# Kernel optimization log

Hardware: AMD Instinct MI355X
Metric: run time of the kernel (lower is better)

Reference implementation:

```python
import jax, jax.numpy as jnp
import numpy as np

NUM_NODES = 5000
NUM_COLORS = 20
NODE_FEAT = 4
COLOR_FEAT = 3
COMBINED = NODE_FEAT + COLOR_FEAT  # 7
HIDDEN = 128
N_GRAPH = NUM_NODES * NUM_COLORS   # 100000 GCN nodes (batch=1)
N_EDGES = 1_600_000


def setup_inputs() -> dict:
    key = jax.random.key(0)
    ks = jax.random.split(key, 12)
    flat_obs = jax.random.normal(ks[0], (1, 3 + NUM_NODES * NODE_FEAT + NUM_COLORS * COLOR_FEAT), dtype=jnp.float32)
    edge_index = jax.random.randint(ks[1], (2, N_EDGES), 0, N_GRAPH, dtype=jnp.int64)
    s = lambda k, sh, fan: jax.random.normal(k, sh, dtype=jnp.float32) / np.sqrt(fan)
    return {
        "flat_obs": flat_obs,
        "edge_index": edge_index,
        "W1": s(ks[2], (COMBINED, HIDDEN), COMBINED),
        "b1": jnp.zeros((HIDDEN,), jnp.float32),
        "W2": s(ks[3], (HIDDEN, HIDDEN), HIDDEN),
        "b2": jnp.zeros((HIDDEN,), jnp.float32),
        "fc1_w": s(ks[4], (HIDDEN, HIDDEN), HIDDEN),
        "fc1_b": jnp.zeros((HIDDEN,), jnp.float32),
        "fc2_w": s(ks[5], (HIDDEN, 1), HIDDEN),
        "fc2_b": jnp.zeros((1,), jnp.float32),
    }


def _gcn_conv(x, W, b, src, dst, norm):
    # PyG GCNConv: out[dst] += norm * (x @ W)[src]; self-loops already in src/dst.
    xw = x @ W                                   # [N, H]
    msg = xw[src] * norm[:, None]                # [E+N, H]
    out = jax.ops.segment_sum(msg, dst, num_segments=N_GRAPH)
    return out + b


def reference(flat_obs, edge_index, W1, b1, W2, b2, fc1_w, fc1_b, fc2_w, fc2_b):
    B = flat_obs.shape[0]
    nf_start = 3
    nf_end = nf_start + NUM_NODES * NODE_FEAT
    cf_end = nf_end + NUM_COLORS * COLOR_FEAT
    node_features = flat_obs[:, nf_start:nf_end].reshape(B, NUM_NODES, NODE_FEAT)
    color_features = flat_obs[:, nf_end:cf_end].reshape(B, NUM_COLORS, COLOR_FEAT)

    # cross-expand: [B, nodes, colors, 4+3]
    en = jnp.broadcast_to(node_features[:, :, None, :], (B, NUM_NODES, NUM_COLORS, NODE_FEAT))
    ec = jnp.broadcast_to(color_features[:, None, :, :], (B, NUM_NODES, NUM_COLORS, COLOR_FEAT))
    combined = jnp.concatenate([en, ec], axis=3).reshape(-1, COMBINED)  # [N_GRAPH, 7]

    # add self loops + symmetric normalization (GCN)
    loops = jnp.arange(N_GRAPH, dtype=edge_index.dtype)
    src = jnp.concatenate([edge_index[0], loops])
    dst = jnp.concatenate([edge_index[1], loops])
    deg = jax.ops.segment_sum(jnp.ones_like(dst, dtype=jnp.float32), dst, num_segments=N_GRAPH)
    dinv = jnp.where(deg > 0, jax.lax.rsqrt(deg), 0.0)
    norm = dinv[src] * dinv[dst]

    x = jax.nn.relu(_gcn_conv(combined, W1, b1, src, dst, norm))
    x = jax.nn.relu(_gcn_conv(x, W2, b2, src, dst, norm))
    x = jax.nn.relu(x @ fc1_w + fc1_b)
    q = x @ fc2_w + fc2_b                         # [N_GRAPH, 1]
    return q.reshape(B, NUM_NODES * NUM_COLORS)
```

## Files before the change

### kernel.cpp

```cpp
#include <hip/hip_runtime.h>

#define NGRAPH 100000
#define NEDGE  1600000
#define HID    128
#define SCAN_B 512
#define NBLK   ((NGRAPH + SCAN_B - 1) / SCAN_B)
#define TILE   32

__device__ __forceinline__ int e_src(const int* ei, int is64, int e) {
    return is64 ? ei[2 * e] : ei[e];
}
__device__ __forceinline__ int e_dst(const int* ei, int is64, int e) {
    return is64 ? ei[2 * NEDGE + 2 * e] : ei[NEDGE + e];
}

__global__ void k_prep(const float* __restrict__ obs, const int* __restrict__ ei,
                       float* __restrict__ comb, int* __restrict__ deg,
                       int* __restrict__ fill, int* __restrict__ flag) {
    if (blockIdx.x == 0 && threadIdx.x < 64) {
        int v = ei[2 * threadIdx.x + 1];
        unsigned long long b = __ballot(v != 0);
        if (threadIdx.x == 0) flag[0] = (b == 0ull) ? 1 : 0;
    }
    int i = blockIdx.x * blockDim.x + threadIdx.x;
    if (i >= NGRAPH) return;
    int n = i / 20, c = i % 20;
    const float* nf = obs + 3 + n * 4;
    const float* cf = obs + 3 + 20000 + c * 3;
    float* o = comb + i * 7;
    o[0] = nf[0]; o[1] = nf[1]; o[2] = nf[2]; o[3] = nf[3];
    o[4] = cf[0]; o[5] = cf[1]; o[6] = cf[2];
    deg[i] = 0;
    fill[i] = 0;
}

__global__ void k_deg(const int* __restrict__ ei, const int* __restrict__ flag,
                      int* __restrict__ deg) {
    int e = blockIdx.x * blockDim.x + threadIdx.x;
    if (e >= NEDGE) return;
    atomicAdd(&deg[e_dst(ei, flag[0], e)], 1);
}

__global__ void __launch_bounds__(SCAN_B) k_scan1(const int* __restrict__ deg,
                                                  int* __restrict__ rowptr,
                                                  int* __restrict__ sums,
                                                  float* __restrict__ dinv) {
    __shared__ int sh[SCAN_B];
    int t = threadIdx.x;
    int i = blockIdx.x * SCAN_B + t;
    int val = (i < NGRAPH) ? deg[i] : 0;
    if (i < NGRAPH) dinv[i] = rsqrtf((float)(val + 1));
    sh[t] = val;
    __syncthreads();
    for (int o = 1; o < SCAN_B; o <<= 1) {
        int x = (t >= o) ? sh[t - o] : 0;
        __syncthreads();
        sh[t] += x;
        __syncthreads();
    }
    if (i < NGRAPH) rowptr[i] = sh[t] - val;
    if (t == SCAN_B - 1) sums[blockIdx.x] = sh[t];
}

__global__ void __launch_bounds__(256) k_scan2(int* __restrict__ sums) {
    __shared__ int sh[256];
    int t = threadIdx.x;
    int val = (t < NBLK) ? sums[t] : 0;
    sh[t] = val;
    __syncthreads();
    for (int o = 1; o < 256; o <<= 1) {
        int x = (t >= o) ? sh[t - o] : 0;
        __syncthreads();
        sh[t] += x;
        __syncthreads();
    }
    if (t < NBLK) sums[t] = sh[t] - val;
}

__global__ void __launch_bounds__(SCAN_B) k_scan3(int* __restrict__ rowptr,
                                                  const int* __restrict__ sums) {
    int i = blockIdx.x * SCAN_B + threadIdx.x;
    if (i < NGRAPH) rowptr[i] += sums[blockIdx.x];
}

__global__ void k_fill(const int* __restrict__ ei, const int* __restrict__ flag,
                       const float* __restrict__ dinv,
                       const int* __restrict__ rowptr, int* __restrict__ fill,
                       int* __restrict__ csr_src, float* __restrict__ csr_w) {
    int e = blockIdx.x * blockDim.x + threadIdx.x;
    if (e >= NEDGE) return;
    int is64 = flag[0];
    int s = e_src(ei, is64, e);
    int d = e_dst(ei, is64, e);
    int pos = rowptr[d] + atomicAdd(&fill[d], 1);
    csr_src[pos] = s;
    csr_w[pos] = dinv[s] * dinv[d];
}

__global__ void __launch_bounds__(256) k_gcn1(const int* __restrict__ rowptr,
                                              const int* __restrict__ deg,
                                              const int* __restrict__ csr_src,
                                              const float* __restrict__ csr_w,
                                              const float* __restrict__ dinv,
                                              const float* __restrict__ comb,
                                              const float* __restrict__ W1,
                                              const float* __restrict__ b1,
                                              float* __restrict__ x1) {
    __shared__ float agg_s[32][8];
    int g = threadIdx.x >> 3;
    int f = threadIdx.x & 7;
    int d = blockIdx.x * 32 + g;
    if (f < 7) {
        int start = rowptr[d], n = deg[d];
        float acc = 0.0f;
        for (int j = 0; j < n; ++j) {
            int s = csr_src[start + j];
            float w = csr_w[start + j];
            acc += w * comb[s * 7 + f];
        }
        float dv = dinv[d];
        acc += dv * dv * comb[d * 7 + f];
        agg_s[g][f] = acc;
    }
    __syncthreads();
    float a[7];
    #pragma unroll
    for (int q = 0; q < 7; ++q) a[q] = agg_s[g][q];
    int h0 = f * 16;
    #pragma unroll
    for (int j = 0; j < 4; ++j) {
        int h = h0 + j * 4;
        float4 acc4 = *reinterpret_cast<const float4*>(b1 + h);
        #pragma unroll
        for (int q = 0; q < 7; ++q) {
            float4 w = *reinterpret_cast<const float4*>(W1 + q * HID + h);
            acc4.x += a[q] * w.x;
            acc4.y += a[q] * w.y;
            acc4.z += a[q] * w.z;
            acc4.w += a[q] * w.w;
        }
        acc4.x = fmaxf(acc4.x, 0.0f); acc4.y = fmaxf(acc4.y, 0.0f);
        acc4.z = fmaxf(acc4.z, 0.0f); acc4.w = fmaxf(acc4.w, 0.0f);
        *reinterpret_cast<float4*>(x1 + (size_t)d * HID + h) = acc4;
    }
}

__global__ void __launch_bounds__(256) k_agg2(const int* __restrict__ rowptr,
                                              const int* __restrict__ deg,
                                              const int* __restrict__ csr_src,
                                              const float* __restrict__ csr_w,
                                              const float* __restrict__ dinv,
                                              const float* __restrict__ x1,
                                              float* __restrict__ agg2) {
    int wave = threadIdx.x >> 6;
    int lane = threadIdx.x & 63;
    int d = blockIdx.x * 4 + wave;
    int f0 = lane * 2;
    int start = rowptr[d], n = deg[d];
    float2 acc = {0.0f, 0.0f};
    int j = 0;
    for (; j + 2 <= n; j += 2) {
        int s0 = csr_src[start + j];
        int s1 = csr_src[start + j + 1];
        float w0 = csr_w[start + j];
        float w1 = csr_w[start + j + 1];
        float2 v0 = *reinterpret_cast<const float2*>(x1 + (size_t)s0 * HID + f0);
        float2 v1 = *reinterpret_cast<const float2*>(x1 + (size_t)s1 * HID + f0);
        acc.x += w0 * v0.x + w1 * v1.x;
        acc.y += w0 * v0.y + w1 * v1.y;
    }
    if (j < n) {
        int s0 = csr_src[start + j];
        float w0 = csr_w[start + j];
        float2 v0 = *reinterpret_cast<const float2*>(x1 + (size_t)s0 * HID + f0);
        acc.x += w0 * v0.x;
        acc.y += w0 * v0.y;
    }
    float dv = dinv[d];
    float ws = dv * dv;
    float2 v = *reinterpret_cast<const float2*>(x1 + (size_t)d * HID + f0);
    acc.x += ws * v.x;
    acc.y += ws * v.y;
    *reinterpret_cast<float2*>(agg2 + (size_t)d * HID + f0) = acc;
}

__device__ __forceinline__ void fma4(float4& acc, const float4 a,
                                     const float4 w0, const float4 w1,
                                     const float4 w2, const float4 w3) {
    acc.x += a.x * w0.x + a.y * w1.x + a.z * w2.x + a.w * w3.x;
    acc.y += a.x * w0.y + a.y * w1.y + a.z * w2.y + a.w * w3.y;
    acc.z += a.x * w0.z + a.y * w1.z + a.z * w2.z + a.w * w3.z;
    acc.w += a.x * w0.w + a.y * w1.w + a.z * w2.w + a.w * w3.w;
}
__device__ __forceinline__ float4 relu4(float4 v) {
    float4 r;
    r.x = fmaxf(v.x, 0.0f); r.y = fmaxf(v.y, 0.0f);
    r.z = fmaxf(v.z, 0.0f); r.w = fmaxf(v.w, 0.0f);
    return r;
}

__global__ void __launch_bounds__(256) k_mlp(const float* __restrict__ agg2,
                                             const float* __restrict__ W2,
                                             const float* __restrict__ b2,
                                             const float* __restrict__ fc1w,
                                             const float* __restrict__ fc1b,
                                             const float* __restrict__ fc2w,
                                             const float* __restrict__ fc2b,
                                             float* __restrict__ out) {
    __shared__ float as_[TILE][HID + 4];
    __shared__ float ws[32][HID + 4];
    const int tid = threadIdx.x;
    const int tx = tid & 31;
    const int ty = tid >> 5;
    const int n0 = blockIdx.x * TILE;
    const int h0 = tx * 4;

    {
        const float* src = agg2 + (size_t)n0 * HID;
        #pragma unroll
        for (int q = 0; q < 4; ++q) {
            int idx = (q * 256 + tid) * 4;
            int row = idx >> 7, col = idx & 127;
            *reinterpret_cast<float4*>(&as_[row][col]) =
                *reinterpret_cast<const float4*>(src + idx);
        }
    }

    float4 bias = *reinterpret_cast<const float4*>(b2 + h0);
    float4 c0 = bias, c1 = bias, c2 = bias, c3 = bias;
    for (int ks = 0; ks < HID; ks += 32) {
        const float* wsrc = W2 + (size_t)ks * HID;
        #pragma unroll
        for (int q = 0; q < 4; ++q) {
            int idx = (q * 256 + tid) * 4;
            int row = idx >> 7, col = idx & 127;
            *reinterpret_cast<float4*>(&ws[row][col]) =
                *reinterpret_cast<const float4*>(wsrc + idx);
        }
        __syncthreads();
        #pragma unroll 4
        for (int k = 0; k < 32; k += 4) {
            float4 w0 = *reinterpret_cast<const float4*>(&ws[k + 0][h0]);
            float4 w1 = *reinterpret_cast<const float4*>(&ws[k + 1][h0]);
            float4 w2 = *reinterpret_cast<const float4*>(&ws[k + 2][h0]);
            float4 w3 = *reinterpret_cast<const float4*>(&ws[k + 3][h0]);
            float4 a0 = *reinterpret_cast<const float4*>(&as_[ty * 4 + 0][ks + k]);
            float4 a1 = *reinterpret_cast<const float4*>(&as_[ty * 4 + 1][ks + k]);
            float4 a2 = *reinterpret_cast<const float4*>(&as_[ty * 4 + 2][ks + k]);
            float4 a3 = *reinterpret_cast<const float4*>(&as_[ty * 4 + 3][ks + k]);
            fma4(c0, a0, w0, w1, w2, w3);
            fma4(c1, a1, w0, w1, w2, w3);
            fma4(c2, a2, w0, w1, w2, w3);
            fma4(c3, a3, w0, w1, w2, w3);
        }
        __syncthreads();
    }
    *reinterpret_cast<float4*>(&as_[ty * 4 + 0][h0]) = relu4(c0);
    *reinterpret_cast<float4*>(&as_[ty * 4 + 1][h0]) = relu4(c1);
    *reinterpret_cast<float4*>(&as_[ty * 4 + 2][h0]) = relu4(c2);
    *reinterpret_cast<float4*>(&as_[ty * 4 + 3][h0]) = relu4(c3);

    float4 bias1 = *reinterpret_cast<const float4*>(fc1b + h0);
    float4 d0 = bias1, d1 = bias1, d2 = bias1, d3 = bias1;
    for (int ks = 0; ks < HID; ks += 32) {
        const float* wsrc = fc1w + (size_t)ks * HID;
        #pragma unroll
        for (int q = 0; q < 4; ++q) {
            int idx = (q * 256 + tid) * 4;
            int row = idx >> 7, col = idx & 127;
            *reinterpret_cast<float4*>(&ws[row][col]) =
                *reinterpret_cast<const float4*>(wsrc + idx);
        }
        __syncthreads();
        #pragma unroll 4
        for (int k = 0; k < 32; k += 4) {
            float4 w0 = *reinterpret_cast<const float4*>(&ws[k + 0][h0]);
            float4 w1 = *reinterpret_cast<const float4*>(&ws[k + 1][h0]);
            float4 w2 = *reinterpret_cast<const float4*>(&ws[k + 2][h0]);
            float4 w3 = *reinterpret_cast<const float4*>(&ws[k + 3][h0]);
            float4 a0 = *reinterpret_cast<const float4*>(&as_[ty * 4 + 0][ks + k]);
            float4 a1 = *reinterpret_cast<const float4*>(&as_[ty * 4 + 1][ks + k]);
            float4 a2 = *reinterpret_cast<const float4*>(&as_[ty * 4 + 2][ks + k]);
            float4 a3 = *reinterpret_cast<const float4*>(&as_[ty * 4 + 3][ks + k]);
            fma4(d0, a0, w0, w1, w2, w3);
            fma4(d1, a1, w0, w1, w2, w3);
            fma4(d2, a2, w0, w1, w2, w3);
            fma4(d3, a3, w0, w1, w2, w3);
        }
        __syncthreads();
    }

    float4 wq = *reinterpret_cast<const float4*>(fc2w + h0);
    float4 r0 = relu4(d0), r1 = relu4(d1), r2 = relu4(d2), r3 = relu4(d3);
    float p0 = r0.x * wq.x + r0.y * wq.y + r0.z * wq.z + r0.w * wq.w;
    float p1 = r1.x * wq.x + r1.y * wq.y + r1.z * wq.z + r1.w * wq.w;
    float p2 = r2.x * wq.x + r2.y * wq.y + r2.z * wq.z + r2.w * wq.w;
    float p3 = r3.x * wq.x + r3.y * wq.y + r3.z * wq.z + r3.w * wq.w;
    #pragma unroll
    for (int m = 1; m < 32; m <<= 1) {
        p0 += __shfl_xor(p0, m);
        p1 += __shfl_xor(p1, m);
        p2 += __shfl_xor(p2, m);
        p3 += __shfl_xor(p3, m);
    }
    if (tx == 0) {
        float bq = fc2b[0];
        int nb = n0 + ty * 4;
        out[nb + 0] = p0 + bq;
        out[nb + 1] = p1 + bq;
        out[nb + 2] = p2 + bq;
        out[nb + 3] = p3 + bq;
    }
}

extern "C" void kernel_launch(void* const* d_in, const int* in_sizes, int n_in,
                              void* d_out, int out_size, void* d_ws, size_t ws_size,
                              hipStream_t stream) {
    const float* obs  = (const float*)d_in[0];
    const int*   ei   = (const int*)d_in[1];
    const float* W1   = (const float*)d_in[2];
    const float* b1   = (const float*)d_in[3];
    const float* W2   = (const float*)d_in[4];
    const float* b2   = (const float*)d_in[5];
    const float* fc1w = (const float*)d_in[6];
    const float* fc1b = (const float*)d_in[7];
    const float* fc2w = (const float*)d_in[8];
    const float* fc2b = (const float*)d_in[9];
    float* out = (float*)d_out;

    char* base = (char*)d_ws;
    size_t off = 0;
    auto take = [&](size_t bytes) {
        char* p = base + off;
        off += (bytes + 255) & ~(size_t)255;
        return p;
    };
    int*   deg     = (int*)take((size_t)NGRAPH * 4);
    int*   rowptr  = (int*)take((size_t)NGRAPH * 4);
    int*   fill    = (int*)take((size_t)NGRAPH * 4);
    int*   sums    = (int*)take((size_t)NBLK * 4);
    float* dinv    = (float*)take((size_t)NGRAPH * 4);
    int*   csr_src = (int*)take((size_t)NEDGE * 4);
    float* csr_w   = (float*)take((size_t)NEDGE * 4);
    float* comb    = (float*)take((size_t)NGRAPH * 7 * 4);
    float* x1      = (float*)take((size_t)NGRAPH * HID * 4);
    float* agg2    = (float*)take((size_t)NGRAPH * HID * 4);
    int*   flag    = (int*)take(256);

    k_prep<<<(NGRAPH + 255) / 256, 256, 0, stream>>>(obs, ei, comb, deg, fill, flag);
    k_deg<<<(NEDGE + 255) / 256, 256, 0, stream>>>(ei, flag, deg);
    k_scan1<<<NBLK, SCAN_B, 0, stream>>>(deg, rowptr, sums, dinv);
    k_scan2<<<1, 256, 0, stream>>>(sums);
    k_scan3<<<NBLK, SCAN_B, 0, stream>>>(rowptr, sums);
    k_fill<<<(NEDGE + 255) / 256, 256, 0, stream>>>(ei, flag, dinv, rowptr, fill,
                                                    csr_src, csr_w);
    k_gcn1<<<NGRAPH / 32, 256, 0, stream>>>(rowptr, deg, csr_src, csr_w, dinv,
                                            comb, W1, b1, x1);
    k_agg2<<<NGRAPH / 4, 256, 0, stream>>>(rowptr, deg, csr_src, csr_w, dinv,
                                           x1, agg2);
    k_mlp<<<NGRAPH / TILE, 256, 0, stream>>>(agg2, W2, b2, fc1w, fc1b,
                                             fc2w, fc2b, out);
}
```

Measured before the change: 546.2 us.

## Interleave CSR src/weight into int2 and retile MLP kernel to 64 rows

Packs each edge's source index and normalization weight into a single int2, so the gather loops in both aggregation kernels issue one 8-byte load per edge instead of two scattered 4-byte loads. The MLP kernel now processes 64 rows per block, with each thread computing 8 output columns for 4 rows, to raise register-level reuse of the shared-memory weight tiles. It also sets a launch-bounds occupancy hint and adds tail guards. The cost is more registers and shared memory per block, which could lower occupancy.

```diff
diff --git a/kernel.cpp b/kernel.cpp
--- a/kernel.cpp
+++ b/kernel.cpp
@@ -5,7 +5,7 @@
 #define HID    128
 #define SCAN_B 512
 #define NBLK   ((NGRAPH + SCAN_B - 1) / SCAN_B)
-#define TILE   32
+#define TILE   64
 
 __device__ __forceinline__ int e_src(const int* ei, int is64, int e) {
     return is64 ? ei[2 * e] : ei[e];
@@ -86,21 +86,19 @@
 __global__ void k_fill(const int* __restrict__ ei, const int* __restrict__ flag,
                        const float* __restrict__ dinv,
                        const int* __restrict__ rowptr, int* __restrict__ fill,
-                       int* __restrict__ csr_src, float* __restrict__ csr_w) {
+                       int2* __restrict__ csr) {
     int e = blockIdx.x * blockDim.x + threadIdx.x;
     if (e >= NEDGE) return;
     int is64 = flag[0];
     int s = e_src(ei, is64, e);
     int d = e_dst(ei, is64, e);
     int pos = rowptr[d] + atomicAdd(&fill[d], 1);
-    csr_src[pos] = s;
-    csr_w[pos] = dinv[s] * dinv[d];
+    csr[pos] = make_int2(s, __float_as_int(dinv[s] * dinv[d]));
 }
 
 __global__ void __launch_bounds__(256) k_gcn1(const int* __restrict__ rowptr,
                                               const int* __restrict__ deg,
-                                              const int* __restrict__ csr_src,
-                                              const float* __restrict__ csr_w,
+                                              const int2* __restrict__ csr,
                                               const float* __restrict__ dinv,
                                               const float* __restrict__ comb,
                                               const float* __restrict__ W1,
@@ -114,9 +112,8 @@
         int start = rowptr[d], n = deg[d];
         float acc = 0.0f;
         for (int j = 0; j < n; ++j) {
-            int s = csr_src[start + j];
-            float w = csr_w[start + j];
-            acc += w * comb[s * 7 + f];
+            int2 ed = csr[start + j];
+            acc += __int_as_float(ed.y) * comb[ed.x * 7 + f];
         }
         float dv = dinv[d];
         acc += dv * dv * comb[d * 7 + f];
@@ -134,10 +131,10 @@
         #pragma unroll
         for (int q = 0; q < 7; ++q) {
             float4 w = *reinterpret_cast<const float4*>(W1 + q * HID + h);
-            acc4.x += a[q] * w.x;
-            acc4.y += a[q] * w.y;
-            acc4.z += a[q] * w.z;
-            acc4.w += a[q] * w.w;
+            acc4.x = fmaf(a[q], w.x, acc4.x);
+            acc4.y = fmaf(a[q], w.y, acc4.y);
+            acc4.z = fmaf(a[q], w.z, acc4.z);
+            acc4.w = fmaf(a[q], w.w, acc4.w);
         }
         acc4.x = fmaxf(acc4.x, 0.0f); acc4.y = fmaxf(acc4.y, 0.0f);
         acc4.z = fmaxf(acc4.z, 0.0f); acc4.w = fmaxf(acc4.w, 0.0f);
@@ -147,8 +144,7 @@
 
 __global__ void __launch_bounds__(256) k_agg2(const int* __restrict__ rowptr,
                                               const int* __restrict__ deg,
-                                              const int* __restrict__ csr_src,
-                                              const float* __restrict__ csr_w,
+                                              const int2* __restrict__ csr,
                                               const float* __restrict__ dinv,
                                               const float* __restrict__ x1,
                                               float* __restrict__ agg2) {
@@ -160,19 +156,19 @@
     float2 acc = {0.0f, 0.0f};
     int j = 0;
     for (; j + 2 <= n; j += 2) {
-        int s0 = csr_src[start + j];
-        int s1 = csr_src[start + j + 1];
-        float w0 = csr_w[start + j];
-        float w1 = csr_w[start + j + 1];
-        float2 v0 = *reinterpret_cast<const float2*>(x1 + (size_t)s0 * HID + f0);
-        float2 v1 = *reinterpret_cast<const float2*>(x1 + (size_t)s1 * HID + f0);
+        int2 e0 = csr[start + j];
+        int2 e1 = csr[start + j + 1];
+        float w0 = __int_as_float(e0.y);
+        float w1 = __int_as_float(e1.y);
+        float2 v0 = *reinterpret_cast<const float2*>(x1 + (size_t)e0.x * HID + f0);
+        float2 v1 = *reinterpret_cast<const float2*>(x1 + (size_t)e1.x * HID + f0);
         acc.x += w0 * v0.x + w1 * v1.x;
         acc.y += w0 * v0.y + w1 * v1.y;
     }
     if (j < n) {
-        int s0 = csr_src[start + j];
-        float w0 = csr_w[start + j];
-        float2 v0 = *reinterpret_cast<const float2*>(x1 + (size_t)s0 * HID + f0);
+        int2 e0 = csr[start + j];
+        float w0 = __int_as_float(e0.y);
+        float2 v0 = *reinterpret_cast<const float2*>(x1 + (size_t)e0.x * HID + f0);
         acc.x += w0 * v0.x;
         acc.y += w0 * v0.y;
     }
@@ -184,13 +180,11 @@
     *reinterpret_cast<float2*>(agg2 + (size_t)d * HID + f0) = acc;
 }
 
-__device__ __forceinline__ void fma4(float4& acc, const float4 a,
-                                     const float4 w0, const float4 w1,
-                                     const float4 w2, const float4 w3) {
-    acc.x += a.x * w0.x + a.y * w1.x + a.z * w2.x + a.w * w3.x;
-    acc.y += a.x * w0.y + a.y * w1.y + a.z * w2.y + a.w * w3.y;
-    acc.z += a.x * w0.z + a.y * w1.z + a.z * w2.z + a.w * w3.z;
-    acc.w += a.x * w0.w + a.y * w1.w + a.z * w2.w + a.w * w3.w;
+__device__ __forceinline__ void fmad(float4& acc, float s, const float4 w) {
+    acc.x = fmaf(s, w.x, acc.x);
+    acc.y = fmaf(s, w.y, acc.y);
+    acc.z = fmaf(s, w.z, acc.z);
+    acc.w = fmaf(s, w.w, acc.w);
 }
 __device__ __forceinline__ float4 relu4(float4 v) {
     float4 r;
@@ -199,117 +193,133 @@
     return r;
 }
 
-__global__ void __launch_bounds__(256) k_mlp(const float* __restrict__ agg2,
-                                             const float* __restrict__ W2,
-                                             const float* __restrict__ b2,
-                                             const float* __restrict__ fc1w,
-                                             const float* __restrict__ fc1b,
-                                             const float* __restrict__ fc2w,
-                                             const float* __restrict__ fc2b,
-                                             float* __restrict__ out) {
+__global__ void __launch_bounds__(256, 3) k_mlp(const float* __restrict__ agg2,
+                                                const float* __restrict__ W2,
+                                                const float* __restrict__ b2,
+                                                const float* __restrict__ fc1w,
+                                                const float* __restrict__ fc1b,
+                                                const float* __restrict__ fc2w,
+                                                const float* __restrict__ fc2b,
+                                                float* __restrict__ out) {
     __shared__ float as_[TILE][HID + 4];
     __shared__ float ws[32][HID + 4];
     const int tid = threadIdx.x;
-    const int tx = tid & 31;
-    const int ty = tid >> 5;
+    const int tx = tid & 15;
+    const int ty = tid >> 4;
     const int n0 = blockIdx.x * TILE;
-    const int h0 = tx * 4;
-
+    const int h0 = tx * 8;
+
+    #pragma unroll
+    for (int q = 0; q < 8; ++q) {
+        int idx = (q * 256 + tid) * 4;
+        int row = idx >> 7, col = idx & 127;
+        int nr = n0 + row; if (nr >= NGRAPH) nr = NGRAPH - 1;
+        *reinterpret_cast<float4*>(&as_[row][col]) =
+            *reinterpret_cast<const float4*>(agg2 + (size_t)nr * HID + col);
+    }
+
+    float4 cA[4], cB[4];
     {
-        const float* src = agg2 + (size_t)n0 * HID;
-        #pragma unroll
-        for (int q = 0; q < 4; ++q) {
-            int idx = (q * 256 + tid) * 4;
-            int row = idx >> 7, col = idx & 127;
-            *reinterpret_cast<float4*>(&as_[row][col]) =
-                *reinterpret_cast<const float4*>(src + idx);
-        }
-    }
-
-    float4 bias = *reinterpret_cast<const float4*>(b2 + h0);
-    float4 c0 = bias, c1 = bias, c2 = bias, c3 = bias;
+        float4 bA = *reinterpret_cast<const float4*>(b2 + h0);
+        float4 bB = *reinterpret_cast<const float4*>(b2 + h0 + 4);
+        #pragma unroll
+        for (int r = 0; r < 4; ++r) { cA[r] = bA; cB[r] = bB; }
+    }
     for (int ks = 0; ks < HID; ks += 32) {
-        const float* wsrc = W2 + (size_t)ks * HID;
         #pragma unroll
         for (int q = 0; q < 4; ++q) {
             int idx = (q * 256 + tid) * 4;
             int row = idx >> 7, col = idx & 127;
             *reinterpret_cast<float4*>(&ws[row][col]) =
-                *reinterpret_cast<const float4*>(wsrc + idx);
-        }
-        __syncthreads();
-        #pragma unroll 4
+                *reinterpret_cast<const float4*>(W2 + (size_t)(ks + row) * HID + col);
+        }
+        __syncthreads();
+        #pragma unroll
         for (int k = 0; k < 32; k += 4) {
-            float4 w0 = *reinterpret_cast<const float4*>(&ws[k + 0][h0]);
-            float4 w1 = *reinterpret_cast<const float4*>(&ws[k + 1][h0]);
-            float4 w2 = *reinterpret_cast<const float4*>(&ws[k + 2][h0]);
-            float4 w3 = *reinterpret_cast<const float4*>(&ws[k + 3][h0]);
-            float4 a0 = *reinterpret_cast<const float4*>(&as_[ty * 4 + 0][ks + k]);
-            float4 a1 = *reinterpret_cast<const float4*>(&as_[ty * 4 + 1][ks + k]);
-            float4 a2 = *reinterpret_cast<const float4*>(&as_[ty * 4 + 2][ks + k]);
-            float4 a3 = *reinterpret_cast<const float4*>(&as_[ty * 4 + 3][ks + k]);
-            fma4(c0, a0, w0, w1, w2, w3);
-            fma4(c1, a1, w0, w1, w2, w3);
-            fma4(c2, a2, w0, w1, w2, w3);
-            fma4(c3, a3, w0, w1, w2, w3);
-        }
-        __syncthreads();
-    }
-    *reinterpret_cast<float4*>(&as_[ty * 4 + 0][h0]) = relu4(c0);
-    *reinterpret_cast<float4*>(&as_[ty * 4 + 1][h0]) = relu4(c1);
-    *reinterpret_cast<float4*>(&as_[ty * 4 + 2][h0]) = relu4(c2);
-    *reinterpret_cast<float4*>(&as_[ty * 4 + 3][h0]) = relu4(c3);
-
-    float4 bias1 = *reinterpret_cast<const float4*>(fc1b + h0);
-    float4 d0 = bias1, d1 = bias1, d2 = bias1, d3 = bias1;
+            float4 wA0 = *reinterpret_cast<const float4*>(&ws[k + 0][h0]);
+            float4 wB0 = *reinterpret_cast<const float4*>(&ws[k + 0][h0 + 4]);
+            float4 wA1 = *reinterpret_cast<const float4*>(&ws[k + 1][h0]);
+            float4 wB1 = *reinterpret_cast<const float4*>(&ws[k + 1][h0 + 4]);
+            float4 wA2 = *reinterpret_cast<const float4*>(&ws[k + 2][h0]);
+            float4 wB2 = *reinterpret_cast<const float4*>(&ws[k + 2][h0 + 4]);
+            float4 wA3 = *reinterpret_cast<const float4*>(&ws[k + 3][h0]);
+            float4 wB3 = *reinterpret_cast<const float4*>(&ws[k + 3][h0 + 4]);
+            #pragma unroll
+            for (int r = 0; r < 4; ++r) {
+                float4 a = *reinterpret_cast<const float4*>(&as_[ty * 4 + r][ks + k]);
+                fmad(cA[r], a.x, wA0); fmad(cB[r], a.x, wB0);
+                fmad(cA[r], a.y, wA1); fmad(cB[r], a.y, wB1);
+                fmad(cA[r], a.z, wA2); fmad(cB[r], a.z, wB2);
+                fmad(cA[r], a.w, wA3); fmad(cB[r], a.w, wB3);
+            }
+        }
+        __syncthreads();
+    }
+    #pragma unroll
+    for (int r = 0; r < 4; ++r) {
+        *reinterpret_cast<float4*>(&as_[ty * 4 + r][h0])     = relu4(cA[r]);
+        *reinterpret_cast<float4*>(&as_[ty * 4 + r][h0 + 4]) = relu4(cB[r]);
+    }
+
+    float4 dA[4], dB[4];
+    {
+        float4 bA = *reinterpret_cast<const float4*>(fc1b + h0);
+        float4 bB = *reinterpret_cast<const float4*>(fc1b + h0 + 4);
+        #pragma unroll
+        for (int r = 0; r < 4; ++r) { dA[r] = bA; dB[r] = bB; }
+    }
     for (int ks = 0; ks < HID; ks += 32) {
-        const float* wsrc = fc1w + (size_t)ks * HID;
         #pragma unroll
         for (int q = 0; q < 4; ++q) {
             int idx = (q * 256 + tid) * 4;
             int row = idx >> 7, col = idx & 127;
             *reinterpret_cast<float4*>(&ws[row][col]) =
-                *reinterpret_cast<const float4*>(wsrc + idx);
-        }
-        __syncthreads();
-        #pragma unroll 4
+                *reinterpret_cast<const float4*>(fc1w + (size_t)(ks + row) * HID + col);
+        }
+        __syncthreads();
+        #pragma unroll
         for (int k = 0; k < 32; k += 4) {
-            float4 w0 = *reinterpret_cast<const float4*>(&ws[k + 0][h0]);
-            float4 w1 = *reinterpret_cast<const float4*>(&ws[k + 1][h0]);
-            float4 w2 = *reinterpret_cast<const float4*>(&ws[k + 2][h0]);
-            float4 w3 = *reinterpret_cast<const float4*>(&ws[k + 3][h0]);
-            float4 a0 = *reinterpret_cast<const float4*>(&as_[ty * 4 + 0][ks + k]);
-            float4 a1 = *reinterpret_cast<const float4*>(&as_[ty * 4 + 1][ks + k]);
-            float4 a2 = *reinterpret_cast<const float4*>(&as_[ty * 4 + 2][ks + k]);
-            float4 a3 = *reinterpret_cast<const float4*>(&as_[ty * 4 + 3][ks + k]);
-            fma4(d0, a0, w0, w1, w2, w3);
-            fma4(d1, a1, w0, w1, w2, w3);
-            fma4(d2, a2, w0, w1, w2, w3);
-            fma4(d3, a3, w0, w1, w2, w3);
-        }
-        __syncthreads();
-    }
-
-    float4 wq = *reinterpret_cast<const float4*>(fc2w + h0);
-    float4 r0 = relu4(d0), r1 = relu4(d1), r2 = relu4(d2), r3 = relu4(d3);
-    float p0 = r0.x * wq.x + r0.y * wq.y + r0.z * wq.z + r0.w * wq.w;
-    float p1 = r1.x * wq.x + r1.y * wq.y + r1.z * wq.z + r1.w * wq.w;
-    float p2 = r2.x * wq.x + r2.y * wq.y + r2.z * wq.z + r2.w * wq.w;
-    float p3 = r3.x * wq.x + r3.y * wq.y + r3.z * wq.z + r3.w * wq.w;
-    #pragma unroll
-    for (int m = 1; m < 32; m <<= 1) {
-        p0 += __shfl_xor(p0, m);
-        p1 += __shfl_xor(p1, m);
-        p2 += __shfl_xor(p2, m);
-        p3 += __shfl_xor(p3, m);
+            float4 wA0 = *reinterpret_cast<const float4*>(&ws[k + 0][h0]);
+            float4 wB0 = *reinterpret_cast<const float4*>(&ws[k + 0][h0 + 4]);
+            float4 wA1 = *reinterpret_cast<const float4*>(&ws[k + 1][h0]);
+            float4 wB1 = *reinterpret_cast<const float4*>(&ws[k + 1][h0 + 4]);
+            float4 wA2 = *reinterpret_cast<const float4*>(&ws[k + 2][h0]);
+            float4 wB2 = *reinterpret_cast<const float4*>(&ws[k + 2][h0 + 4]);
+            float4 wA3 = *reinterpret_cast<const float4*>(&ws[k + 3][h0]);
+            float4 wB3 = *reinterpret_cast<const float4*>(&ws[k + 3][h0 + 4]);
+            #pragma unroll
+            for (int r = 0; r < 4; ++r) {
+                float4 a = *reinterpret_cast<const float4*>(&as_[ty * 4 + r][ks + k]);
+                fmad(dA[r], a.x, wA0); fmad(dB[r], a.x, wB0);
+                fmad(dA[r], a.y, wA1); fmad(dB[r], a.y, wB1);
+                fmad(dA[r], a.z, wA2); fmad(dB[r], a.z, wB2);
+                fmad(dA[r], a.w, wA3); fmad(dB[r], a.w, wB3);
+            }
+        }
+        __syncthreads();
+    }
+
+    float4 wqA = *reinterpret_cast<const float4*>(fc2w + h0);
+    float4 wqB = *reinterpret_cast<const float4*>(fc2w + h0 + 4);
+    float p[4];
+    #pragma unroll
+    for (int r = 0; r < 4; ++r) {
+        float4 rA = relu4(dA[r]);
+        float4 rB = relu4(dB[r]);
+        p[r] = rA.x * wqA.x + rA.y * wqA.y + rA.z * wqA.z + rA.w * wqA.w
+             + rB.x * wqB.x + rB.y * wqB.y + rB.z * wqB.z + rB.w * wqB.w;
+    }
+    #pragma unroll
+    for (int m = 1; m < 16; m <<= 1) {
+        #pragma unroll
+        for (int r = 0; r < 4; ++r) p[r] += __shfl_xor(p[r], m);
     }
     if (tx == 0) {
         float bq = fc2b[0];
         int nb = n0 + ty * 4;
-        out[nb + 0] = p0 + bq;
-        out[nb + 1] = p1 + bq;
-        out[nb + 2] = p2 + bq;
-        out[nb + 3] = p3 + bq;
+        #pragma unroll
+        for (int r = 0; r < 4; ++r)
+            if (nb + r < NGRAPH) out[nb + r] = p[r] + bq;
     }
 }
 
@@ -340,8 +350,7 @@
     int*   fill    = (int*)take((size_t)NGRAPH * 4);
     int*   sums    = (int*)take((size_t)NBLK * 4);
     float* dinv    = (float*)take((size_t)NGRAPH * 4);
-    int*   csr_src = (int*)take((size_t)NEDGE * 4);
-    float* csr_w   = (float*)take((size_t)NEDGE * 4);
+    int2*  csr     = (int2*)take((size_t)NEDGE * 8);
     float* comb    = (float*)take((size_t)NGRAPH * 7 * 4);
     float* x1      = (float*)take((size_t)NGRAPH * HID * 4);
     float* agg2    = (float*)take((size_t)NGRAPH * HID * 4);
@@ -352,12 +361,11 @@
     k_scan1<<<NBLK, SCAN_B, 0, stream>>>(deg, rowptr, sums, dinv);
     k_scan2<<<1, 256, 0, stream>>>(sums);
     k_scan3<<<NBLK, SCAN_B, 0, stream>>>(rowptr, sums);
-    k_fill<<<(NEDGE + 255) / 256, 256, 0, stream>>>(ei, flag, dinv, rowptr, fill,
-                                                    csr_src, csr_w);
-    k_gcn1<<<NGRAPH / 32, 256, 0, stream>>>(rowptr, deg, csr_src, csr_w, dinv,
+    k_fill<<<(NEDGE + 255) / 256, 256, 0, stream>>>(ei, flag, dinv, rowptr, fill, csr);
+    k_gcn1<<<NGRAPH / 32, 256, 0, stream>>>(rowptr, deg, csr, dinv,
                                             comb, W1, b1, x1);
-    k_agg2<<<NGRAPH / 4, 256, 0, stream>>>(rowptr, deg, csr_src, csr_w, dinv,
-                                           x1, agg2);
-    k_mlp<<<NGRAPH / TILE, 256, 0, stream>>>(agg2, W2, b2, fc1w, fc1b,
-                                             fc2w, fc2b, out);
-}
+    k_agg2<<<NGRAPH / 4, 256, 0, stream>>>(rowptr, deg, csr, dinv, x1, agg2);
+    k_mlp<<<(NGRAPH + TILE - 1) / TILE, 256, 0, stream>>>(agg2, W2, b2,
+                                                          fc1w, fc1b,
+                                                          fc2w, fc2b, out);
+}
```

After: 501.8 us. 8.1% less time.
